# Kernel tuning notes

Hardware: AMD Instinct MI355X
Metric: run time of the kernel (lower is better)

The kernel has to match this reference:

```python
import jax, jax.numpy as jnp
import numpy as np

N = 50000; E = 800000; G = 256
FIN = 64; EIN = 16; HC = 128; H = 2; C = 64; EF = 64; NB = 2
EPS = 1e-5
SQRT_C = np.float32(np.sqrt(C))


def elu(x):
    return jax.nn.elu(x)


def seg_softmax(logits, seg, num):
    # numerically stable softmax over groups defined by seg
    m = jax.ops.segment_max(logits, seg, num_segments=num)
    e = jnp.exp(logits - m[seg])
    s = jax.ops.segment_sum(e, seg, num_segments=num)
    return e / s[seg]


def graph_ln(x, batch, gamma, beta):
    # PyG LayerNorm(mode='graph'): stats over all nodes AND channels of each graph
    cnt = jax.ops.segment_sum(jnp.ones((x.shape[0],), x.dtype), batch, num_segments=G) * x.shape[1]
    cnt = jnp.maximum(cnt, 1.0)
    s = jax.ops.segment_sum(x.sum(-1), batch, num_segments=G)
    ss = jax.ops.segment_sum((x * x).sum(-1), batch, num_segments=G)
    mean = s / cnt
    var = jnp.maximum(ss / cnt - mean * mean, 0.0)
    xn = (x - mean[batch][:, None]) * jax.lax.rsqrt(var + EPS)[batch][:, None]
    return xn * gamma + beta


def tconv(x, ea, src, dst, wq, bq, wk, bk, wv, bv, we, wsk, bsk):
    # PyG TransformerConv (concat=True, beta=False, root_weight=True, dropout=0)
    q = (x @ wq + bq).reshape(N, H, C)
    k = (x @ wk + bk).reshape(N, H, C)
    v = (x @ wv + bv).reshape(N, H, C)
    e = (ea @ we).reshape(E, H, C)
    kj = k[src] + e
    alpha = jnp.einsum('ehc,ehc->eh', q[dst], kj) / SQRT_C
    alpha = seg_softmax(alpha, dst, N)  # scatter-softmax over destination nodes
    out = jax.ops.segment_sum((v[src] + e) * alpha[:, :, None], dst, num_segments=N)
    return out.reshape(N, HC) + x @ wsk + bsk


def setup_inputs():
    key = jax.random.key(0)
    ks = jax.random.split(key, 16)
    rn = lambda k, shape, sc: jax.random.normal(k, shape, jnp.float32) * sc
    s64 = 1.0 / np.sqrt(64.0); s128 = 1.0 / np.sqrt(128.0); s16 = 1.0 / np.sqrt(16.0)
    return {
        'x': rn(ks[0], (N, FIN), 1.0),
        'edge_attr': rn(ks[1], (E, EIN), 1.0),
        'edge_index': jax.random.randint(ks[2], (2, E), 0, N, jnp.int32),
        'batch': jnp.sort(jax.random.randint(ks[3], (N,), 0, G, jnp.int32)),
        'w0': rn(ks[4], (FIN, HC), s64), 'b0': jnp.zeros((HC,), jnp.float32),
        'we0': rn(ks[5], (EIN, EF), s16), 'be0': jnp.zeros((EF,), jnp.float32),
        'ln0_g': jnp.ones((HC,), jnp.float32), 'ln0_b': jnp.zeros((HC,), jnp.float32),
        'qkv_w': rn(ks[6], (NB, 2, 3, HC, HC), s128), 'qkv_b': jnp.zeros((NB, 2, 3, HC), jnp.float32),
        'edge_w': rn(ks[7], (NB, 2, EF, HC), s64),
        'skip_w': rn(ks[8], (NB, 2, HC, HC), s128), 'skip_b': jnp.zeros((NB, 2, HC), jnp.float32),
        'up_w': rn(ks[9], (NB, 2, EF, EF), s64), 'up_b': jnp.zeros((NB, 2, EF), jnp.float32),
        'ng': jnp.ones((NB, 2, HC), jnp.float32), 'nb': jnp.zeros((NB, 2, HC), jnp.float32),
        'sag_wrel': rn(ks[10], (NB, HC), s128), 'sag_brel': jnp.zeros((NB,), jnp.float32),
        'sag_wroot': rn(ks[11], (NB, HC), s128),
        're_w': rn(ks[12], (NB, EF, HC), s64), 're_b': jnp.zeros((NB, HC), jnp.float32),
    }


def reference(x, edge_attr, edge_index, batch, w0, b0, we0, be0, ln0_g, ln0_b,
              qkv_w, qkv_b, edge_w, skip_w, skip_b, up_w, up_b, ng, nb,
              sag_wrel, sag_brel, sag_wroot, re_w, re_b):
    src, dst = edge_index[0], edge_index[1]
    h = elu(graph_ln(x @ w0 + b0, batch, ln0_g, ln0_b))
    ea = elu(edge_attr @ we0 + be0)
    embs = []
    for i in range(NB):
        # ne_update: conv1 + graph-LN + lin_up on edges
        h = tconv(h, ea, src, dst,
                  qkv_w[i, 0, 0], qkv_b[i, 0, 0], qkv_w[i, 0, 1], qkv_b[i, 0, 1],
                  qkv_w[i, 0, 2], qkv_b[i, 0, 2], edge_w[i, 0], skip_w[i, 0], skip_b[i, 0])
        h = elu(graph_ln(h, batch, ng[i, 0], nb[i, 0]))
        ea = elu(ea @ up_w[i, 0] + up_b[i, 0])
        # conv2 + lin_up2
        h = tconv(h, ea, src, dst,
                  qkv_w[i, 1, 0], qkv_b[i, 1, 0], qkv_w[i, 1, 1], qkv_b[i, 1, 1],
                  qkv_w[i, 1, 2], qkv_b[i, 1, 2], edge_w[i, 1], skip_w[i, 1], skip_b[i, 1])
        ea2 = ea @ up_w[i, 1] + up_b[i, 1]
        # SAGPooling(min_score=-1) keeps all nodes: score = per-graph softmax of GraphConv
        aggr = jax.ops.segment_sum(h[src], dst, num_segments=N)
        sc = aggr @ sag_wrel[i] + sag_brel[i] + h @ sag_wroot[i]  # [N]
        sc = seg_softmax(sc, batch, G)
        emb = jax.ops.segment_sum(h * sc[:, None], batch, num_segments=G)
        emb_e = elu(jax.ops.segment_sum(ea2, batch[src], num_segments=G) @ re_w[i] + re_b[i])
        emb = emb * emb_e
        emb = elu(emb / jnp.maximum(jnp.linalg.norm(emb, axis=1, keepdims=True), 1e-12))
        embs.append(emb)
        h = elu(graph_ln(h, batch, ng[i, 1], nb[i, 1]))
        ea = elu(ea2)
    return 0.6 * embs[0] + 0.4 * embs[-1]
```

## Files before the change

### kernel.cpp

```cpp
#include <hip/hip_runtime.h>
#include <math.h>

#define NN 50000
#define EE 800000
#define GG 256

typedef unsigned short u16;
typedef unsigned int u32;
typedef __attribute__((ext_vector_type(4))) float f32x4;
typedef __attribute__((ext_vector_type(8))) short bf16x8;

__device__ __forceinline__ float elu_f(float x) { return x > 0.f ? x : expm1f(x); }

__device__ __forceinline__ unsigned fenc(float f) {
  unsigned b = __float_as_uint(f);
  return (b & 0x80000000u) ? ~b : (b | 0x80000000u);
}
__device__ __forceinline__ float fdec(unsigned u) {
  return __uint_as_float((u & 0x80000000u) ? (u ^ 0x80000000u) : ~u);
}
__device__ __forceinline__ u16 f2b(float f) {
  u32 u = __float_as_uint(f);
  u32 r = (u + 0x7fffu + ((u >> 16) & 1u)) >> 16;
  return (u16)r;
// ... 90 lines not shown
  s[t] = v;
  __syncthreads();
  for (int off = 1; off < 256; off <<= 1) {
    int tmp = (t >= off) ? s[t - off] : 0;
    __syncthreads();
    s[t] += tmp;
    __syncthreads();
  }
  if (t < nb) bsum[t] = s[t] - v;
}

__global__ void scan3(const int* __restrict__ pre, const int* __restrict__ bsum,
                      const int* __restrict__ deg, int* __restrict__ row_start,
                      int* __restrict__ cursor, int n) {
  int i = blockIdx.x * 256 + threadIdx.x;
  if (i < n) {
    int v = pre[i] + bsum[blockIdx.x];
    row_start[i] = v;
    cursor[i] = v;
    if (i == n - 1) row_start[n] = v + deg[i];
  }
}

__global__ void gstart_build(const int* __restrict__ batch, int* __restrict__ gstart) {
  int n = blockIdx.x * blockDim.x + threadIdx.x;
  if (n > NN) return;
  int b = (n < NN) ? batch[n] : GG;
  int pb = (n == 0) ? -1 : batch[n - 1];
  for (int g = pb + 1; g <= b; ++g) gstart[g] = n;
}

__global__ void csr_pos(const int* __restrict__ src, const int* __restrict__ dst,
                        int* __restrict__ cursor, int* __restrict__ csr_src,
                        int* __restrict__ epos) {
  int e = blockIdx.x * blockDim.x + threadIdx.x;
  if (e >= EE) return;
  int pos = atomicAdd(&cursor[dst[e]], 1);
  csr_src[pos] = src[e];
  epos[e] = pos;
}

__global__ void out_hist(const int* __restrict__ csr_src, int* __restrict__ odeg) {
  int pos = blockIdx.x * blockDim.x + threadIdx.x;
  if (pos < EE) atomicAdd(&odeg[csr_src[pos]], 1);
}

__global__ void out_fill(const int* __restrict__ csr_src, int* __restrict__ ocursor,
                         int* __restrict__ operm) {
  int pos = blockIdx.x * blockDim.x + threadIdx.x;
  if (pos < EE) {
    int slot = atomicAdd(&ocursor[csr_src[pos]], 1);
    operm[slot] = pos;
  }
}

__global__ void sgstart_build(const int* __restrict__ out_start, const int* __restrict__ gstart,
                              int* __restrict__ sg_start) {
  int t = blockIdx.x * blockDim.x + threadIdx.x;
  if (t <= GG) sg_start[t] = out_start[gstart[t]];
}

__global__ void build_we0frag(const float* __restrict__ we0, u16* __restrict__ wf_hi,
                              u16* __restrict__ wf_lo) {
  int idx = blockIdx.x * 256 + threadIdx.x;
  if (idx >= 2048) return;
  int j = idx & 7, lane = (idx >> 3) & 63, t = idx >> 9;
  int k = (lane >> 4) * 8 + j;
  int c = t * 16 + (lane & 15);
  float w = (k < 16) ? we0[(size_t)k * 64 + c] : 0.f;
  u16 hi = f2b(w);
  wf_hi[idx] = hi;
  wf_lo[idx] = f2b(w - bf2f(hi));
}

__global__ __launch_bounds__(256) void ea_enc_mfma(const float* __restrict__ edge_attr,
                                                   const u16* __restrict__ wf_hi,
                                                   const u16* __restrict__ wf_lo,
                                                   const float* __restrict__ be0,
                                                   const int* __restrict__ epos,
                                                   u16* __restrict__ ea) {
  int lane = threadIdx.x & 63;
  int gwave = (blockIdx.x * 256 + threadIdx.x) >> 6;
  int nwaves = (gridDim.x * 256) >> 6;
  bf16x8 bh[4], bl[4];
#pragma unroll
  for (int t = 0; t < 4; ++t) {
    bh[t] = *reinterpret_cast<const bf16x8*>(wf_hi + ((size_t)(t * 64 + lane)) * 8);
    bl[t] = *reinterpret_cast<const bf16x8*>(wf_lo + ((size_t)(t * 64 + lane)) * 8);
  }
  float bias_c[4];
#pragma unroll
  for (int t = 0; t < 4; ++t) bias_c[t] = be0[t * 16 + (lane & 15)];
  const int rif = lane & 15;
  const int kg = lane >> 4;
  for (int mt = gwave; mt < EE / 16; mt += nwaves) {
    int base = mt * 16;
    bf16x8 ah = {}, al = {};
    if (kg < 2) {
      const float* ap = edge_attr + (size_t)(base + rif) * 16 + kg * 8;
      float4 f0 = *reinterpret_cast<const float4*>(ap);
      float4 f1 = *reinterpret_cast<const float4*>(ap + 4);
      float fv[8] = {f0.x, f0.y, f0.z, f0.w, f1.x, f1.y, f1.z, f1.w};
#pragma unroll
      for (int jj = 0; jj < 8; ++jj) {
        u16 hi = f2b(fv[jj]);
        ah[jj] = (short)hi;
        al[jj] = (short)f2b(fv[jj] - bf2f(hi));
      }
    }
    f32x4 acc[4] = {};
#pragma unroll
    for (int t = 0; t < 4; ++t) {
      acc[t] = __builtin_amdgcn_mfma_f32_16x16x32_bf16(ah, bh[t], acc[t], 0, 0, 0);
      acc[t] = __builtin_amdgcn_mfma_f32_16x16x32_bf16(ah, bl[t], acc[t], 0, 0, 0);
      acc[t] = __builtin_amdgcn_mfma_f32_16x16x32_bf16(al, bh[t], acc[t], 0, 0, 0);
    }
#pragma unroll
    for (int rg = 0; rg < 4; ++rg) {
      int pr = epos[base + kg * 4 + rg];
#pragma unroll
      for (int t = 0; t < 4; ++t)
        ea[(size_t)pr * 64 + t * 16 + rif] = f2b(elu_f(acc[t][rg] + bias_c[t]));
    }
  }
}

__global__ __launch_bounds__(256) void ln_stats_block(const float* __restrict__ h,
                                                      const int* __restrict__ gstart,
                                                      float* __restrict__ gmean,
                                                      float* __restrict__ grstd) {
  __shared__ float ls[4], lss[4];
  int g = blockIdx.x, t = threadIdx.x;
  int n0 = gstart[g], n1 = gstart[g + 1];
  int total4 = (n1 - n0) * 32;
  const float4* base = (const float4*)(h + (size_t)n0 * 128);
  float s = 0.f, ss = 0.f;
  for (int i = t; i < total4; i += 256) {
    float4 v = base[i];
    s += v.x + v.y + v.z + v.w;
    ss += v.x * v.x + v.y * v.y + v.z * v.z + v.w * v.w;
  }
  s = wred64(s);
  ss = wred64(ss);
  if ((t & 63) == 0) { ls[t >> 6] = s; lss[t >> 6] = ss; }
  __syncthreads();
  if (t == 0) {
    float S = ls[0] + ls[1] + ls[2] + ls[3];
    float SS = lss[0] + lss[1] + lss[2] + lss[3];
    float cnt = fmaxf((float)(n1 - n0) * 128.f, 1.0f);
    float mean = S / cnt;
    float var = fmaxf(SS / cnt - mean * mean, 0.f);
    gmean[g] = mean;
    grstd[g] = rsqrtf(var + 1e-5f);
  }
}

__global__ __launch_bounds__(256) void ln_apply(const float* __restrict__ in,
                                                u16* __restrict__ out_hi,
                                                u16* __restrict__ out_lo,
                                                const int* __restrict__ batch,
                                                const float* __restrict__ gmean,
                                                const float* __restrict__ grstd,
                                                const float* __restrict__ gamma,
                                                const float* __restrict__ beta) {
  int idx = blockIdx.x * blockDim.x + threadIdx.x;
  if (idx >= NN * 32) return;
  int n = idx >> 5, c4 = (idx & 31) * 4;
  int g = batch[n];
  float mean = gmean[g], rstd = grstd[g];
  float4 xv = *reinterpret_cast<const float4*>(in + (size_t)n * 128 + c4);
  float4 gv = *reinterpret_cast<const float4*>(gamma + c4);
  float4 bv = *reinterpret_cast<const float4*>(beta + c4);
  float v0 = elu_f((xv.x - mean) * rstd * gv.x + bv.x);
  float v1 = elu_f((xv.y - mean) * rstd * gv.y + bv.y);
  float v2 = elu_f((xv.z - mean) * rstd * gv.z + bv.z);
  float v3 = elu_f((xv.w - mean) * rstd * gv.w + bv.w);
  u16 h0 = f2b(v0), h1 = f2b(v1), h2 = f2b(v2), h3 = f2b(v3);
  uint2 hi = {(u32)h0 | ((u32)h1 << 16), (u32)h2 | ((u32)h3 << 16)};
  uint2 lo = {(u32)f2b(v0 - bf2f(h0)) | ((u32)f2b(v1 - bf2f(h1)) << 16),
              (u32)f2b(v2 - bf2f(h2)) | ((u32)f2b(v3 - bf2f(h3)) << 16)};
  *reinterpret_cast<uint2*>(out_hi + (size_t)n * 128 + c4) = hi;
  *reinterpret_cast<uint2*>(out_lo + (size_t)n * 128 + c4) = lo;
}

__global__ void build_wqe(const float* __restrict__ wq, const float* __restrict__ bq,
                          const float* __restrict__ we, float* __restrict__ WQE,
                          float* __restrict__ bqe) {
  int col = threadIdx.x;
  int row = blockIdx.x;
  int hh = col >> 6, j = col & 63;
  const float* wrow = (row < 128) ? (wq + (size_t)row * 128) : bq;
  float acc = 0.f;
  for (int c = 0; c < 64; ++c) acc += wrow[hh * 64 + c] * we[(size_t)j * 128 + hh * 64 + c];
  if (row < 128) WQE[(size_t)row * 128 + col] = acc;
  else bqe[col] = acc;
}

__global__ void build_wfrag2(const float* __restrict__ wq, const float* __restrict__ wk,
                             const float* __restrict__ wv, const float* __restrict__ WQE,
                             const float* __restrict__ wsk,
                             const float* __restrict__ bq, const float* __restrict__ bk,
                             const float* __restrict__ bv, const float* __restrict__ bqe,
                             const float* __restrict__ bsk,
                             u16* __restrict__ Wfrag_hi, u16* __restrict__ Wfrag_lo,
                             float* __restrict__ ball) {
  int idx = blockIdx.x * 256 + threadIdx.x;
  if (idx < 81920) {
    int j = idx & 7, lane = (idx >> 3) & 63, rest = idx >> 9;
    int tg = rest % 40, s = rest / 40;
    int k = s * 32 + (lane >> 4) * 8 + j;
    int col = tg * 16 + (lane & 15);
    int sel = col >> 7, c = col & 127;
    const float* src = sel == 0 ? wq : sel == 1 ? wk : sel == 2 ? wv : sel == 3 ? WQE : wsk;
    float w = src[(size_t)k * 128 + c];
    u16 hi = f2b(w);
    Wfrag_hi[idx] = hi;
    Wfrag_lo[idx] = f2b(w - bf2f(hi));
  }
  if (idx < 640) {
    int sel = idx >> 7, c = idx & 127;
    const float* s2 = sel == 0 ? bq : sel == 1 ? bk : sel == 2 ? bv : sel == 3 ? bqe : bsk;
    ball[idx] = s2[c];
  }
}

__global__ void build_wefrag(const float* __restrict__ we, u16* __restrict__ wef_hi,
                             u16* __restrict__ wef_lo) {
  int idx = blockIdx.x * 256 + threadIdx.x;
  if (idx >= 8192) return;
  int j = idx & 7, lane = (idx >> 3) & 63, rest = idx >> 9;
  int t = rest & 3, hh = (rest >> 2) & 1, s = rest >> 3;
  int k = s * 32 + (lane >> 4) * 8 + j;
  int col = hh * 64 + t * 16 + (lane & 15);
  float w = we[(size_t)k * 128 + col];
  u16 hi = f2b(w);
  wef_hi[idx] = hi;
  wef_lo[idx] = f2b(w - bf2f(hi));
}

__global__ void build_upfrag(const float* __restrict__ up, u16* __restrict__ upfrag) {
  int idx = blockIdx.x * 256 + threadIdx.x;
  if (idx >= 4096) return;
  int j = idx & 7, lane = (idx >> 3) & 63, st = idx >> 9;
  int s = st >> 2, t = st & 3;
  int k = s * 32 + (lane >> 4) * 8 + j;
  int c = t * 16 + (lane & 15);
  upfrag[idx] = f2b(up[k * 64 + c]);
}

__global__ void build_w2(const float* __restrict__ up, const float* __restrict__ ub,
                         const float* __restrict__ re_w, float* __restrict__ W2,
                         float* __restrict__ bvec) {
  int idx = blockIdx.x * 256 + threadIdx.x;
  if (idx < 64 * 128) {
    int k_ = idx >> 7, c = idx & 127;
    float a = 0.f;
    for (int j = 0; j < 64; ++j) a = fmaf(up[k_ * 64 + j], re_w[j * 128 + c], a);
    W2[idx] = a;
  } else if (idx < 64 * 128 + 128) {
    int c = idx - 64 * 128;
    float a = 0.f;
    for (int j = 0; j < 64; ++j) a = fmaf(ub[j], re_w[j * 128 + c], a);
    bvec[c] = a;
  }
}

__global__ __launch_bounds__(256) void node_gemm(const u16* __restrict__ h_hi,
                                                 const u16* __restrict__ h_lo,
                                                 const u16* __restrict__ Wfrag_hi,
                                                 const u16* __restrict__ Wfrag_lo,
                                                 const float* __restrict__ ball,
                                                 u16* __restrict__ nodebuf,
                                                 float* __restrict__ hn) {
  int tid = threadIdx.x;
  int lane = tid & 63;
  int wv = tid >> 6;
  int cb = blockIdx.x;
  int rbase = blockIdx.y * 64 + wv * 16;
  int rif = lane & 15, kg = lane >> 4;
  f32x4 acc[4] = {};
  int arow = rbase + rif;
  bool rowok = arow < NN;
  const u16* aph = h_hi + (size_t)arow * 128 + kg * 8;
  const u16* apl = h_lo + (size_t)arow * 128 + kg * 8;
#pragma unroll
  for (int s = 0; s < 4; ++s) {
    bf16x8 ah = {}, al = {};
    if (rowok) {
      ah = *reinterpret_cast<const bf16x8*>(aph + s * 32);
      al = *reinterpret_cast<const bf16x8*>(apl + s * 32);
    }
#pragma unroll
    for (int t = 0; t < 4; ++t) {
      size_t fo = ((size_t)((s * 40 + cb * 4 + t) * 64 + lane)) * 8;
      bf16x8 bh = *reinterpret_cast<const bf16x8*>(Wfrag_hi + fo);
      bf16x8 bl = *reinterpret_cast<const bf16x8*>(Wfrag_lo + fo);
      acc[t] = __builtin_amdgcn_mfma_f32_16x16x32_bf16(ah, bh, acc[t], 0, 0, 0);
      acc[t] = __builtin_amdgcn_mfma_f32_16x16x32_bf16(ah, bl, acc[t], 0, 0, 0);
      acc[t] = __builtin_amdgcn_mfma_f32_16x16x32_bf16(al, bh, acc[t], 0, 0, 0);
    }
  }
#pragma unroll
  for (int t = 0; t < 4; ++t) {
    int col = (cb * 4 + t) * 16 + rif;
    float bia = ball[col];
#pragma unroll
    for (int rg = 0; rg < 4; ++rg) {
      int row = rbase + kg * 4 + rg;
      if (row < NN) {
        float val = acc[t][rg] + bia;
        if (col < 512) {
          int idx;
          if (col < 128) idx = col;
          else if (col < 256) { int c1 = col - 128; idx = 256 + ((c1 >> 1) << 2) + (c1 & 1); }
          else if (col < 384) { int c2 = col - 256; idx = 256 + ((c2 >> 1) << 2) + 2 + (c2 & 1); }
          else idx = 128 + (col - 384);
          nodebuf[(size_t)row * 512 + idx] = f2b(val);
        } else {
          hn[(size_t)row * 128 + col - 512] = val;
        }
      }
    }
  }
}

__global__ __launch_bounds__(256) void edge_gemm(u16* __restrict__ ea,
                                                 const u16* __restrict__ upfrag,
                                                 const float* __restrict__ ub) {
  int lane = threadIdx.x & 63;
  int gwave = (blockIdx.x * 256 + threadIdx.x) >> 6;
  int nwaves = (gridDim.x * 256) >> 6;
  bf16x8 bfrag[2][4];
#pragma unroll
  for (int s = 0; s < 2; ++s)
#pragma unroll
    for (int t = 0; t < 4; ++t)
      bfrag[s][t] = *reinterpret_cast<const bf16x8*>(upfrag + ((size_t)((s * 4 + t) * 64 + lane)) * 8);
  float bias_c[4];
#pragma unroll
  for (int t = 0; t < 4; ++t) bias_c[t] = ub[t * 16 + (lane & 15)];
  const int rif = lane & 15;
  const int kg = lane >> 4;
  for (int mt = gwave; mt < EE / 16; mt += nwaves) {
    size_t rowbase = (size_t)mt * 16;
    const u16* arow = ea + (rowbase + rif) * 64;
    bf16x8 a0 = *reinterpret_cast<const bf16x8*>(arow + kg * 8);
    bf16x8 a1 = *reinterpret_cast<const bf16x8*>(arow + 32 + kg * 8);
    f32x4 acc[4] = {};
#pragma unroll
    for (int t = 0; t < 4; ++t) {
      acc[t] = __builtin_amdgcn_mfma_f32_16x16x32_bf16(a0, bfrag[0][t], acc[t], 0, 0, 0);
      acc[t] = __builtin_amdgcn_mfma_f32_16x16x32_bf16(a1, bfrag[1][t], acc[t], 0, 0, 0);
    }
#pragma unroll
    for (int t = 0; t < 4; ++t)
#pragma unroll
      for (int rg = 0; rg < 4; ++rg) {
        float val = acc[t][rg] + bias_c[t];
        ea[(rowbase + kg * 4 + rg) * 64 + t * 16 + rif] = f2b(elu_f(val));
      }
  }
}

__global__ __launch_bounds__(256) void bd_gemm(const u16* __restrict__ r_hi,
                                               const u16* __restrict__ r_lo,
                                               const u16* __restrict__ wef_hi,
                                               const u16* __restrict__ wef_lo,
                                               float* __restrict__ hn) {
  int tid = threadIdx.x;
  int lane = tid & 63;
  int w = blockIdx.x * 4 + (tid >> 6);
  if (w >= NN / 16) return;
  int rif = lane & 15, kg = lane >> 4;
  size_t rowbase = (size_t)w * 16;
  const u16* ahb = r_hi + (rowbase + rif) * 128;
  const u16* alb = r_lo + (rowbase + rif) * 128;
  f32x4 acc[2][4] = {};
#pragma unroll
  for (int hh = 0; hh < 2; ++hh)
#pragma unroll
    for (int s = 0; s < 2; ++s) {
      int ko = hh * 64 + s * 32 + kg * 8;
      bf16x8 ah = *reinterpret_cast<const bf16x8*>(ahb + ko);
      bf16x8 al = *reinterpret_cast<const bf16x8*>(alb + ko);
#pragma unroll
      for (int t = 0; t < 4; ++t) {
        size_t fo = ((size_t)((((s * 2 + hh) * 4 + t)) * 64 + lane)) * 8;
        bf16x8 bh = *reinterpret_cast<const bf16x8*>(wef_hi + fo);
        bf16x8 bl = *reinterpret_cast<const bf16x8*>(wef_lo + fo);
        acc[hh][t] = __builtin_amdgcn_mfma_f32_16x16x32_bf16(ah, bh, acc[hh][t], 0, 0, 0);
        acc[hh][t] = __builtin_amdgcn_mfma_f32_16x16x32_bf16(ah, bl, acc[hh][t], 0, 0, 0);
        acc[hh][t] = __builtin_amdgcn_mfma_f32_16x16x32_bf16(al, bh, acc[hh][t], 0, 0, 0);
      }
    }
#pragma unroll
  for (int hh = 0; hh < 2; ++hh)
#pragma unroll
    for (int t = 0; t < 4; ++t)
#pragma unroll
      for (int rg = 0; rg < 4; ++rg) {
        size_t row = rowbase + kg * 4 + rg;
        int col = hh * 64 + t * 16 + rif;
        hn[row * 128 + col] += acc[hh][t][rg];
      }
}

__global__ __launch_bounds__(256) void gsum_pre(const u16* __restrict__ ea,
                                                const int* __restrict__ sg_start,
                                                const int* __restrict__ sg_perm,
                                                float* __restrict__ gsum_in) {
  __shared__ float red[8][64];
  int g = blockIdx.x, t = threadIdx.x;
  int c2 = t & 31;
  int rgrp = t >> 5;
  int gr = blockIdx.y * 8 + rgrp;
  int p0 = sg_start[g], p1 = sg_start[g + 1];
  float slo = 0.f, shi = 0.f;
  for (int i = p0 + gr; i < p1; i += 128) {
    int pos = sg_perm[i];
    u32 w = ((const u32*)ea)[(size_t)pos * 32 + c2];
    slo += lo2f(w);
    shi += hi2f(w);
  }
  red[rgrp][c2 * 2] = slo;
  red[rgrp][c2 * 2 + 1] = shi;
  __syncthreads();
  if (t < 64) {
    float a = 0.f;
#pragma unroll
    for (int rr = 0; rr < 8; ++rr) a += red[rr][t];
    atomicAdd(&gsum_in[(size_t)g * 64 + t], a);
  }
}

__global__ void emb_e_kernel(const float* __restrict__ gsum_in, const int* __restrict__ sg_start,
                             const float* __restrict__ W2, const float* __restrict__ bvec,
                             const float* __restrict__ re_b, float* __restrict__ embE) {
  int g = blockIdx.x, c = threadIdx.x;
  float cnt = (float)(sg_start[g + 1] - sg_start[g]);
  float a = re_b[c] + cnt * bvec[c];
  for (int k_ = 0; k_ < 64; ++k_) a = fmaf(gsum_in[(size_t)g * 64 + k_], W2[k_ * 128 + c], a);
  embE[(size_t)g * 128 + c] = elu_f(a);
}

__global__ __launch_bounds__(256) void attn_node(const u32* __restrict__ nodebuf,
                                                 const u16* __restrict__ ea,
                                                 const int* __restrict__ row_start,
                                                 const int* __restrict__ csr_src,
                                                 float* __restrict__ hn,
                                                 u32* __restrict__ r_hi,
                                                 u32* __restrict__ r_lo) {
  int d = (blockIdx.x * blockDim.x + threadIdx.x) >> 6;
  if (d >= NN) return;
  int lane = threadIdx.x & 63;
  int p0 = row_start[d], p1 = row_start[d + 1];
  if (p0 == p1) {
    r_hi[(size_t)d * 64 + lane] = 0u;
    r_lo[(size_t)d * 64 + lane] = 0u;
    return;
  }
  int cnt = p1 - p0;
  size_t dbase = (size_t)d * 256;
  u32 qv = nodebuf[dbase + lane];
  u32 qev = nodebuf[dbase + 64 + lane];
  const int lea = lane & 31;
  float mA = -3.4e38f, sA = 0.f, a0A = 0.f, a1A = 0.f, r0A = 0.f, r1A = 0.f;
  float mB = -3.4e38f, sB = 0.f, a0B = 0.f, a1B = 0.f, r0B = 0.f, r1B = 0.f;
  int sa = csr_src[p0];
  uint2 kvA = *((const uint2*)(nodebuf + (size_t)sa * 256 + 128) + lane);
  u32 eaA = ((const u32*)ea)[(size_t)p0 * 32 + lea];
  int pB0 = (cnt > 1) ? p0 + 1 : p0;
  int sb = csr_src[pB0];
  uint2 kvB = *((const uint2*)(nodebuf + (size_t)sb * 256 + 128) + lane);
  u32 eaB = ((const u32*)ea)[(size_t)pB0 * 32 + lea];
  for (int i = 0; i < cnt; i += 2) {
    int ni = i + 2;
    int nA = (ni < cnt) ? p0 + ni : p0;
    int nB = (ni + 1 < cnt) ? p0 + ni + 1 : p0;
    int sa2 = csr_src[nA];
    uint2 kvA2 = *((const uint2*)(nodebuf + (size_t)sa2 * 256 + 128) + lane);
    u32 eaA2 = ((const u32*)ea)[(size_t)nA * 32 + lea];
    int sb2 = csr_src[nB];
    uint2 kvB2 = *((const uint2*)(nodebuf + (size_t)sb2 * 256 + 128) + lane);
    u32 eaB2 = ((const u32*)ea)[(size_t)nB * 32 + lea];
    float pA = lo2f(qv) * lo2f(kvA.x) + hi2f(qv) * hi2f(kvA.x) +
               lo2f(qev) * lo2f(eaA) + hi2f(qev) * hi2f(eaA);
    float pB = lo2f(qv) * lo2f(kvB.x) + hi2f(qv) * hi2f(kvB.x) +
               lo2f(qev) * lo2f(eaB) + hi2f(qev) * hi2f(eaB);
#pragma unroll
    for (int mm = 16; mm; mm >>= 1) {
      pA += __shfl_xor(pA, mm, 64);
      pB += __shfl_xor(pB, mm, 64);
    }
    {
      float l = pA * 0.125f;
      float mn = fmaxf(mA, l);
      float f = __expf(mA - mn), w = __expf(l - mn);
      sA = sA * f + w;
      a0A = a0A * f + w * lo2f(kvA.y); a1A = a1A * f + w * hi2f(kvA.y);
      r0A = r0A * f + w * lo2f(eaA);   r1A = r1A * f + w * hi2f(eaA);
      mA = mn;
    }
    if (i + 1 < cnt) {
      float l = pB * 0.125f;
      float mn = fmaxf(mB, l);
      float f = __expf(mB - mn), w = __expf(l - mn);
      sB = sB * f + w;
      a0B = a0B * f + w * lo2f(kvB.y); a1B = a1B * f + w * hi2f(kvB.y);
      r0B = r0B * f + w * lo2f(eaB);   r1B = r1B * f + w * hi2f(eaB);
      mB = mn;
    }
    kvA = kvA2; eaA = eaA2; kvB = kvB2; eaB = eaB2;
  }
  float mn = fmaxf(mA, mB);
  float fA = __expf(mA - mn);
  float fB = (cnt > 1) ? __expf(mB - mn) : 0.f;
  float ssum = sA * fA + sB * fB;
  float a0 = a0A * fA + a0B * fB, a1 = a1A * fA + a1B * fB;
  float r0 = r0A * fA + r0B * fB, r1 = r1A * fA + r1B * fB;
  float inv = 1.f / ssum;
  size_t ob = (size_t)d * 128 + lane * 2;
  hn[ob] += a0 * inv;
  hn[ob + 1] += a1 * inv;
  float rv0 = r0 * inv, rv1 = r1 * inv;
  u16 h0 = f2b(rv0), h1 = f2b(rv1);
  r_hi[(size_t)d * 64 + lane] = (u32)h0 | ((u32)h1 << 16);
  r_lo[(size_t)d * 64 + lane] = (u32)f2b(rv0 - bf2f(h0)) | ((u32)f2b(rv1 - bf2f(h1)) << 16);
}

__global__ __launch_bounds__(256) void node_dots(const float* __restrict__ hn,
                                                 const float* __restrict__ wrel,
                                                 const float* __restrict__ wroot,
                                                 float* __restrict__ hrel,
                                                 float* __restrict__ troot) {
  int n = (blockIdx.x * blockDim.x + threadIdx.x) >> 6;
  if (n >= NN) return;
  int lane = threadIdx.x & 63;
  float x0 = hn[(size_t)n * 128 + lane], x1 = hn[(size_t)n * 128 + 64 + lane];
  float tr = wred64(x0 * wrel[lane] + x1 * wrel[64 + lane]);
  float tt = wred64(x0 * wroot[lane] + x1 * wroot[64 + lane]);
  if (lane == 0) { hrel[n] = tr; troot[n] = tt; }
}

__global__ __launch_bounds__(256) void sag_gather(const float* __restrict__ hrel,
                                                  const float* __restrict__ troot,
                                                  const float* __restrict__ brel,
                                                  const int* __restrict__ row_start,
                                                  const int* __restrict__ csr_src,
                                                  const int* __restrict__ batch,
                                                  float* __restrict__ sc, unsigned* __restrict__ gm) {
  int n = blockIdx.x * blockDim.x + threadIdx.x;
  if (n >= NN) return;
  float s = 0.f;
  int p1 = row_start[n + 1];
  for (int pos = row_start[n]; pos < p1; ++pos) s += hrel[csr_src[pos]];
  float v = s + troot[n] + brel[0];
  sc[n] = v;
  atomicMax(&gm[batch[n]], fenc(v));
}

__global__ __launch_bounds__(256) void sag_exp(const float* __restrict__ sc,
                                               const int* __restrict__ batch,
                                               const unsigned* __restrict__ gm,
                                               float* __restrict__ gs, float* __restrict__ scp) {
  int n = blockIdx.x * blockDim.x + threadIdx.x;
  if (n >= NN) return;
  int g = batch[n];
  float p = __expf(sc[n] - fdec(gm[g]));
  scp[n] = p;
  atomicAdd(&gs[g], p);
}

__global__ void emb_block(const float* __restrict__ hn, const float* __restrict__ scp,
                          const float* __restrict__ gs, const int* __restrict__ gstart,
                          const float* __restrict__ embE, float* __restrict__ dstv) {
  __shared__ float part[2];
  int g = blockIdx.x, c = threadIdx.x;
  int n0 = gstart[g], n1 = gstart[g + 1];
  float invg = 1.f / gs[g];
  float acc = 0.f;
  for (int n = n0; n < n1; ++n) acc = fmaf(hn[(size_t)n * 128 + c], scp[n] * invg, acc);
  float val = acc * embE[(size_t)g * 128 + c];
  float sq = val * val;
#pragma unroll
  for (int mm = 32; mm; mm >>= 1) sq += __shfl_xor(sq, mm, 64);
  if ((c & 63) == 0) part[c >> 6] = sq;
  __syncthreads();
  float nrm = sqrtf(part[0] + part[1]);
  dstv[(size_t)g * 128 + c] = elu_f(val / fmaxf(nrm, 1e-12f));
}

__global__ void final_combine(const float* __restrict__ e0, const float* __restrict__ e1,
                              float* __restrict__ out) {
  int idx = blockIdx.x * blockDim.x + threadIdx.x;
  if (idx >= GG * 128) return;
  out[idx] = 0.6f * e0[idx] + 0.4f * e1[idx];
}

extern "C" void kernel_launch(void* const* d_in, const int* in_sizes, int n_in,
                              void* d_out, int out_size, void* d_ws, size_t ws_size,
                              hipStream_t stream) {
  const float* x = (const float*)d_in[0];
  const float* edge_attr = (const float*)d_in[1];
  const int* edge_index = (const int*)d_in[2];
  const int* batch = (const int*)d_in[3];
  const float* w0 = (const float*)d_in[4];
  const float* b0 = (const float*)d_in[5];
  const float* we0 = (const float*)d_in[6];
  const float* be0 = (const float*)d_in[7];
  const float* ln0_g = (const float*)d_in[8];
  const float* ln0_b = (const float*)d_in[9];
  const float* qkv_w = (const float*)d_in[10];
  const float* qkv_b = (const float*)d_in[11];
  const float* edge_w = (const float*)d_in[12];
  const float* skip_w = (const float*)d_in[13];
  const float* skip_b = (const float*)d_in[14];
  const float* up_w = (const float*)d_in[15];
  const float* up_b = (const float*)d_in[16];
  const float* ng = (const float*)d_in[17];
  const float* nbeta = (const float*)d_in[18];
  const float* sag_wrel = (const float*)d_in[19];
  const float* sag_brel = (const float*)d_in[20];
  const float* sag_wroot = (const float*)d_in[21];
  const float* re_w = (const float*)d_in[22];
  const float* re_b = (const float*)d_in[23];
  const int* srcp = edge_index;
  const int* dstp = edge_index + EE;
  float* out = (float*)d_out;
  (void)in_sizes; (void)n_in;

  float* ws = (float*)d_ws;
  size_t o = 0;
  auto alloc = [&](size_t n) { n = (n + 3) & ~(size_t)3; float* p = ws + o; o += n; return p; };
  u16* h_hi = (u16*)alloc((size_t)NN * 64);
  u16* h_lo = (u16*)alloc((size_t)NN * 64);
  float* hn = alloc((size_t)NN * 128);
  u32* r_hi = (u32*)alloc((size_t)NN * 64);
  u32* r_lo = (u32*)alloc((size_t)NN * 64);
  u16* nodebuf = (u16*)alloc((size_t)NN * 256);
  u16* ea = (u16*)alloc((size_t)EE * 32);
  int* csr_src = (int*)alloc(EE);
  int* epos = (int*)alloc(EE);
  int* deg = (int*)alloc(NN);
  int* pre = (int*)alloc(NN);
  int* bsum = (int*)alloc(256);
  int* row_start = (int*)alloc(NN + 1);
  int* cursor = (int*)alloc(NN);
  int* out_start = (int*)alloc(NN + 1);
  int* gstart = (int*)alloc(GG + 1);
  int* sg_perm = (int*)alloc(EE);
  int* sg_start = (int*)alloc(GG + 1);
  float* gsum_in = alloc(GG * 64);
  float* W2 = alloc(64 * 128);
  float* bvec = alloc(128);
  u16* upfrag = (u16*)alloc(2048);
  u16* Wfrag_hi = (u16*)alloc(40960);
  u16* Wfrag_lo = (u16*)alloc(40960);
  u16* wef_hi = (u16*)alloc(4096);
  u16* wef_lo = (u16*)alloc(4096);
  u16* wef0_hi = (u16*)alloc(1024);
  u16* wef0_lo = (u16*)alloc(1024);
  unsigned* gm = (unsigned*)alloc(GG);
  float* gs = alloc(GG);
  float* gmean = alloc(GG);
  float* grstd = alloc(GG);
  float* WQE = alloc(128 * 128);
  float* bqe = alloc(128);
  float* ball = alloc(640);
  float* hrel = alloc(NN);
  float* troot = alloc(NN);
  float* sc = alloc(NN);
  float* scp = alloc(NN);
  float* embE = alloc(GG * 128);
  float* embs0 = alloc(GG * 128);
  float* embs1 = alloc(GG * 128);

  const size_t need = o * sizeof(float);
  if (ws_size < need) {
    hipMemsetAsync(d_out, 0, (size_t)out_size * sizeof(float), stream);
    return;
  }
  const int NSCAN = (NN + 255) / 256;

  auto gemm = [&](const float* A, const float* B, const float* bias, float* C,
                  int M, int Nn, int K, int act, int accum) {
    dim3 g((Nn + 63) / 64, (M + 63) / 64);
    gemm_kernel<<<g, 256, 0, stream>>>(A, B, bias, C, M, Nn, K, act, accum);
  };
  auto ex_scan = [&](const int* degp, int* startp, int* curp) {
    scan1<<<NSCAN, 256, 0, stream>>>(degp, pre, bsum, NN);
    scan2<<<1, 256, 0, stream>>>(bsum, NSCAN);
    scan3<<<NSCAN, 256, 0, stream>>>(pre, bsum, degp, startp, curp, NN);
  };
  auto graph_ln = [&](const float* in, const float* gamma, const float* beta) {
    ln_stats_block<<<GG, 256, 0, stream>>>(in, gstart, gmean, grstd);
    ln_apply<<<NN * 32 / 256, 256, 0, stream>>>(in, h_hi, h_lo, batch, gmean, grstd, gamma, beta);
  };
  auto tconv = [&](int il) {
    const float* wq = qkv_w + (size_t)(il * 3 + 0) * 128 * 128;
    const float* wk = qkv_w + (size_t)(il * 3 + 1) * 128 * 128;
    const float* wv = qkv_w + (size_t)(il * 3 + 2) * 128 * 128;
    const float* bq = qkv_b + (il * 3 + 0) * 128;
    const float* bk = qkv_b + (il * 3 + 1) * 128;
    const float* bv = qkv_b + (il * 3 + 2) * 128;
    const float* we = edge_w + (size_t)il * 64 * 128;
    const float* wsk = skip_w + (size_t)il * 128 * 128;
    const float* bsk = skip_b + il * 128;
    build_wqe<<<129, 128, 0, stream>>>(wq, bq, we, WQE, bqe);
    build_wfrag2<<<320, 256, 0, stream>>>(wq, wk, wv, WQE, wsk, bq, bk, bv, bqe, bsk,
                                          Wfrag_hi, Wfrag_lo, ball);
    build_wefrag<<<32, 256, 0, stream>>>(we, wef_hi, wef_lo);
    dim3 ng2(10, (NN + 63) / 64);
    node_gemm<<<ng2, 256, 0, stream>>>(h_hi, h_lo, Wfrag_hi, Wfrag_lo, ball, nodebuf, hn);
    attn_node<<<NN / 4, 256, 0, stream>>>((const u32*)nodebuf, ea, row_start, csr_src, hn,
                                          r_hi, r_lo);
    bd_gemm<<<(NN / 16 + 3) / 4, 256, 0, stream>>>((const u16*)r_hi, (const u16*)r_lo,
                                                   wef_hi, wef_lo, hn);
  };
  auto ea_mlp = [&](int il) {
    build_upfrag<<<16, 256, 0, stream>>>(up_w + (size_t)il * 4096, upfrag);
    edge_gemm<<<2048, 256, 0, stream>>>(ea, upfrag, up_b + il * 64);
  };

  hipMemsetAsync(deg, 0, NN * sizeof(int), stream);
  csr_hist<<<(EE + 255) / 256, 256, 0, stream>>>(dstp, deg);
  ex_scan(deg, row_start, cursor);
  gstart_build<<<(NN + 256) / 256, 256, 0, stream>>>(batch, gstart);
  csr_pos<<<(EE + 255) / 256, 256, 0, stream>>>(srcp, dstp, cursor, csr_src, epos);
  build_we0frag<<<8, 256, 0, stream>>>(we0, wef0_hi, wef0_lo);
  ea_enc_mfma<<<2048, 256, 0, stream>>>(edge_attr, wef0_hi, wef0_lo, be0, epos, ea);
  hipMemsetAsync(deg, 0, NN * sizeof(int), stream);
  out_hist<<<(EE + 255) / 256, 256, 0, stream>>>(csr_src, deg);
  ex_scan(deg, out_start, cursor);
  out_fill<<<(EE + 255) / 256, 256, 0, stream>>>(csr_src, cursor, sg_perm);
  sgstart_build<<<2, 256, 0, stream>>>(out_start, gstart, sg_start);
  gemm(x, w0, b0, hn, NN, 128, 64, 0, 0);
  graph_ln(hn, ln0_g, ln0_b);

  for (int i = 0; i < 2; ++i) {
    tconv(i * 2 + 0);
    graph_ln(hn, ng + (i * 2) * 128, nbeta + (i * 2) * 128);
    ea_mlp(i * 2);
    tconv(i * 2 + 1);
    hipMemsetAsync(gm, 0, 2 * GG * sizeof(float), stream);
    hipMemsetAsync(gsum_in, 0, GG * 64 * sizeof(float), stream);
    dim3 gsg(GG, 16);
    gsum_pre<<<gsg, 256, 0, stream>>>(ea, sg_start, sg_perm, gsum_in);
    build_w2<<<33, 256, 0, stream>>>(up_w + (size_t)(i * 2 + 1) * 4096,
                                     up_b + (i * 2 + 1) * 64,
                                     re_w + (size_t)i * 64 * 128, W2, bvec);
    if (i == 0) ea_mlp(i * 2 + 1);
    node_dots<<<NN / 4, 256, 0, stream>>>(hn, sag_wrel + i * 128, sag_wroot + i * 128, hrel, troot);
    sag_gather<<<(NN + 255) / 256, 256, 0, stream>>>(hrel, troot, sag_brel + i, row_start,
                                                     csr_src, batch, sc, gm);
    sag_exp<<<(NN + 255) / 256, 256, 0, stream>>>(sc, batch, gm, gs, scp);
    emb_e_kernel<<<GG, 128, 0, stream>>>(gsum_in, sg_start, W2, bvec, re_b + i * 128, embE);
    emb_block<<<GG, 128, 0, stream>>>(hn, scp, gs, gstart, embE, i == 0 ? embs0 : embs1);
    if (i == 0) graph_ln(hn, ng + (i * 2 + 1) * 128, nbeta + (i * 2 + 1) * 128);
  }
  final_combine<<<GG * 128 / 256, 256, 0, stream>>>(embs0, embs1, out);
}
```

Measured before the change: 1.764 ms.

## Fuse graph-norm stats into bd_gemm epilogue and merge setup kernels

```diff
diff --git a/kernel.cpp b/kernel.cpp
--- a/kernel.cpp
+++ b/kernel.cpp
@@ -266,6 +266,18 @@
     float var = fmaxf(SS / cnt - mean * mean, 0.f);
     gmean[g] = mean;
     grstd[g] = rsqrtf(var + 1e-5f);
+  }
+}
+
+__global__ void ln_final2(const float* __restrict__ gstat, const int* __restrict__ gstart,
+                          float* __restrict__ gmean, float* __restrict__ grstd) {
+  int t = threadIdx.x;
+  if (t < GG) {
+    float cnt = fmaxf((float)(gstart[t + 1] - gstart[t]) * 128.f, 1.0f);
+    float mean = gstat[t] / cnt;
+    float var = fmaxf(gstat[GG + t] / cnt - mean * mean, 0.f);
+    gmean[t] = mean;
+    grstd[t] = rsqrtf(var + 1e-5f);
   }
 }
 
@@ -312,12 +324,13 @@
 
 __global__ void build_wfrag2(const float* __restrict__ wq, const float* __restrict__ wk,
                              const float* __restrict__ wv, const float* __restrict__ WQE,
-                             const float* __restrict__ wsk,
+                             const float* __restrict__ wsk, const float* __restrict__ we,
                              const float* __restrict__ bq, const float* __restrict__ bk,
                              const float* __restrict__ bv, const float* __restrict__ bqe,
                              const float* __restrict__ bsk,
                              u16* __restrict__ Wfrag_hi, u16* __restrict__ Wfrag_lo,
-                             float* __restrict__ ball) {
+                             u16* __restrict__ wef_hi, u16* __restrict__ wef_lo,
+                             float* __restrict__ ball, float* __restrict__ gstat) {
   int idx = blockIdx.x * 256 + threadIdx.x;
   if (idx < 81920) {
     int j = idx & 7, lane = (idx >> 3) & 63, rest = idx >> 9;
@@ -330,26 +343,24 @@
     u16 hi = f2b(w);
     Wfrag_hi[idx] = hi;
     Wfrag_lo[idx] = f2b(w - bf2f(hi));
+  } else if (idx < 90112) {
+    int i2 = idx - 81920;
+    int j = i2 & 7, lane = (i2 >> 3) & 63, rest = i2 >> 9;
+    int t = rest & 3, hh = (rest >> 2) & 1, s = rest >> 3;
+    int k = s * 32 + (lane >> 4) * 8 + j;
+    int col = hh * 64 + t * 16 + (lane & 15);
+    float w = we[(size_t)k * 128 + col];
+    u16 hi = f2b(w);
+    wef_hi[i2] = hi;
+    wef_lo[i2] = f2b(w - bf2f(hi));
+  } else if (idx < 90112 + 2 * GG) {
+    gstat[idx - 90112] = 0.f;
   }
   if (idx < 640) {
     int sel = idx >> 7, c = idx & 127;
     const float* s2 = sel == 0 ? bq : sel == 1 ? bk : sel == 2 ? bv : sel == 3 ? bqe : bsk;
     ball[idx] = s2[c];
   }
-}
-
-__global__ void build_wefrag(const float* __restrict__ we, u16* __restrict__ wef_hi,
-                             u16* __restrict__ wef_lo) {
-  int idx = blockIdx.x * 256 + threadIdx.x;
-  if (idx >= 8192) return;
-  int j = idx & 7, lane = (idx >> 3) & 63, rest = idx >> 9;
-  int t = rest & 3, hh = (rest >> 2) & 1, s = rest >> 3;
-  int k = s * 32 + (lane >> 4) * 8 + j;
-  int col = hh * 64 + t * 16 + (lane & 15);
-  float w = we[(size_t)k * 128 + col];
-  u16 hi = f2b(w);
-  wef_hi[idx] = hi;
-  wef_lo[idx] = f2b(w - bf2f(hi));
 }
 
 __global__ void build_upfrag(const float* __restrict__ up, u16* __restrict__ upfrag) {
@@ -364,7 +375,7 @@
 
 __global__ void build_w2(const float* __restrict__ up, const float* __restrict__ ub,
                          const float* __restrict__ re_w, float* __restrict__ W2,
-                         float* __restrict__ bvec) {
+                         float* __restrict__ bvec, float* __restrict__ gsum_in) {
   int idx = blockIdx.x * 256 + threadIdx.x;
   if (idx < 64 * 128) {
     int k_ = idx >> 7, c = idx & 127;
@@ -377,6 +388,7 @@
     for (int j = 0; j < 64; ++j) a = fmaf(ub[j], re_w[j * 128 + c], a);
     bvec[c] = a;
   }
+  if (idx < GG * 64) gsum_in[idx] = 0.f;
 }
 
 __global__ __launch_bounds__(256) void node_gemm(const u16* __restrict__ h_hi,
@@ -480,7 +492,9 @@
                                                const u16* __restrict__ r_lo,
                                                const u16* __restrict__ wef_hi,
                                                const u16* __restrict__ wef_lo,
-                                               float* __restrict__ hn) {
+                                               float* __restrict__ hn,
+                                               const int* __restrict__ batch,
+                                               float* __restrict__ gstat) {
   int tid = threadIdx.x;
   int lane = tid & 63;
   int w = blockIdx.x * 4 + (tid >> 6);
@@ -508,15 +522,30 @@
       }
     }
 #pragma unroll
-  for (int hh = 0; hh < 2; ++hh)
-#pragma unroll
-    for (int t = 0; t < 4; ++t)
-#pragma unroll
-      for (int rg = 0; rg < 4; ++rg) {
-        size_t row = rowbase + kg * 4 + rg;
-        int col = hh * 64 + t * 16 + rif;
-        hn[row * 128 + col] += acc[hh][t][rg];
+  for (int rg = 0; rg < 4; ++rg) {
+    size_t row = rowbase + kg * 4 + rg;
+    float s = 0.f, sq = 0.f;
+#pragma unroll
+    for (int hh = 0; hh < 2; ++hh)
+#pragma unroll
+      for (int t = 0; t < 4; ++t) {
+        size_t off = row * 128 + hh * 64 + t * 16 + rif;
+        float val = hn[off] + acc[hh][t][rg];
+        hn[off] = val;
+        s += val;
+        sq += val * val;
       }
+#pragma unroll
+    for (int mm = 1; mm <= 8; mm <<= 1) {
+      s += __shfl_xor(s, mm, 64);
+      sq += __shfl_xor(sq, mm, 64);
+    }
+    if (rif == 0) {
+      int g = batch[row];
+      atomicAdd(&gstat[g], s);
+      atomicAdd(&gstat[GG + g], sq);
+    }
+  }
 }
 
 __global__ __launch_bounds__(256) void gsum_pre(const u16* __restrict__ ea,
@@ -557,8 +586,8 @@
   embE[(size_t)g * 128 + c] = elu_f(a);
 }
 
-__global__ __launch_bounds__(256) void attn_node(const u32* __restrict__ nodebuf,
-                                                 const u16* __restrict__ ea,
+__global__ __launch_bounds__(256) void attn_node(const u32* __restrict__ nb32,
+                                                 const u32* __restrict__ ea32,
                                                  const int* __restrict__ row_start,
                                                  const int* __restrict__ csr_src,
                                                  float* __restrict__ hn,
@@ -567,87 +596,99 @@
   int d = (blockIdx.x * blockDim.x + threadIdx.x) >> 6;
   if (d >= NN) return;
   int lane = threadIdx.x & 63;
+  int half = lane >> 5;
+  int l = lane & 31;
+  int li = l & 15;
+  int qi = (l >> 4) * 32 + li * 2;
   int p0 = row_start[d], p1 = row_start[d + 1];
   if (p0 == p1) {
-    r_hi[(size_t)d * 64 + lane] = 0u;
-    r_lo[(size_t)d * 64 + lane] = 0u;
+    if (!half) {
+      uint2 z = {0u, 0u};
+      *reinterpret_cast<uint2*>(r_hi + (size_t)d * 64 + qi) = z;
+      *reinterpret_cast<uint2*>(r_lo + (size_t)d * 64 + qi) = z;
+    }
     return;
   }
+  size_t dbase = (size_t)d * 256;
+  uint2 qp = *reinterpret_cast<const uint2*>(nb32 + dbase + qi);
+  uint2 qep = *reinterpret_cast<const uint2*>(nb32 + dbase + 64 + qi);
+  float q0 = lo2f(qp.x), q1 = hi2f(qp.x), q2 = lo2f(qp.y), q3 = hi2f(qp.y);
+  float g0 = lo2f(qep.x), g1 = hi2f(qep.x), g2 = lo2f(qep.y), g3 = hi2f(qep.y);
   int cnt = p1 - p0;
-  size_t dbase = (size_t)d * 256;
-  u32 qv = nodebuf[dbase + lane];
-  u32 qev = nodebuf[dbase + 64 + lane];
-  const int lea = lane & 31;
-  float mA = -3.4e38f, sA = 0.f, a0A = 0.f, a1A = 0.f, r0A = 0.f, r1A = 0.f;
-  float mB = -3.4e38f, sB = 0.f, a0B = 0.f, a1B = 0.f, r0B = 0.f, r1B = 0.f;
-  int sa = csr_src[p0];
-  uint2 kvA = *((const uint2*)(nodebuf + (size_t)sa * 256 + 128) + lane);
-  u32 eaA = ((const u32*)ea)[(size_t)p0 * 32 + lea];
-  int pB0 = (cnt > 1) ? p0 + 1 : p0;
-  int sb = csr_src[pB0];
-  uint2 kvB = *((const uint2*)(nodebuf + (size_t)sb * 256 + 128) + lane);
-  u32 eaB = ((const u32*)ea)[(size_t)pB0 * 32 + lea];
-  for (int i = 0; i < cnt; i += 2) {
-    int ni = i + 2;
-    int nA = (ni < cnt) ? p0 + ni : p0;
-    int nB = (ni + 1 < cnt) ? p0 + ni + 1 : p0;
-    int sa2 = csr_src[nA];
-    uint2 kvA2 = *((const uint2*)(nodebuf + (size_t)sa2 * 256 + 128) + lane);
-    u32 eaA2 = ((const u32*)ea)[(size_t)nA * 32 + lea];
-    int sb2 = csr_src[nB];
-    uint2 kvB2 = *((const uint2*)(nodebuf + (size_t)sb2 * 256 + 128) + lane);
-    u32 eaB2 = ((const u32*)ea)[(size_t)nB * 32 + lea];
-    float pA = lo2f(qv) * lo2f(kvA.x) + hi2f(qv) * hi2f(kvA.x) +
-               lo2f(qev) * lo2f(eaA) + hi2f(qev) * hi2f(eaA);
-    float pB = lo2f(qv) * lo2f(kvB.x) + hi2f(qv) * hi2f(kvB.x) +
-               lo2f(qev) * lo2f(eaB) + hi2f(qev) * hi2f(eaB);
-#pragma unroll
-    for (int mm = 16; mm; mm >>= 1) {
-      pA += __shfl_xor(pA, mm, 64);
-      pB += __shfl_xor(pB, mm, 64);
-    }
-    {
-      float l = pA * 0.125f;
-      float mn = fmaxf(mA, l);
-      float f = __expf(mA - mn), w = __expf(l - mn);
-      sA = sA * f + w;
-      a0A = a0A * f + w * lo2f(kvA.y); a1A = a1A * f + w * hi2f(kvA.y);
-      r0A = r0A * f + w * lo2f(eaA);   r1A = r1A * f + w * hi2f(eaA);
-      mA = mn;
-    }
-    if (i + 1 < cnt) {
-      float l = pB * 0.125f;
-      float mn = fmaxf(mB, l);
-      float f = __expf(mB - mn), w = __expf(l - mn);
-      sB = sB * f + w;
-      a0B = a0B * f + w * lo2f(kvB.y); a1B = a1B * f + w * hi2f(kvB.y);
-      r0B = r0B * f + w * lo2f(eaB);   r1B = r1B * f + w * hi2f(eaB);
-      mB = mn;
-    }
-    kvA = kvA2; eaA = eaA2; kvB = kvB2; eaB = eaB2;
-  }
-  float mn = fmaxf(mA, mB);
-  float fA = __expf(mA - mn);
-  float fB = (cnt > 1) ? __expf(mB - mn) : 0.f;
-  float ssum = sA * fA + sB * fB;
-  float a0 = a0A * fA + a0B * fB, a1 = a1A * fA + a1B * fB;
-  float r0 = r0A * fA + r0B * fB, r1 = r1A * fA + r1B * fB;
-  float inv = 1.f / ssum;
-  size_t ob = (size_t)d * 128 + lane * 2;
-  hn[ob] += a0 * inv;
-  hn[ob + 1] += a1 * inv;
-  float rv0 = r0 * inv, rv1 = r1 * inv;
-  u16 h0 = f2b(rv0), h1 = f2b(rv1);
-  r_hi[(size_t)d * 64 + lane] = (u32)h0 | ((u32)h1 << 16);
-  r_lo[(size_t)d * 64 + lane] = (u32)f2b(rv0 - bf2f(h0)) | ((u32)f2b(rv1 - bf2f(h1)) << 16);
+  int nIter = (cnt + 1) >> 1;
+  float m = -3.4e38f, ss = 0.f;
+  float a0 = 0.f, a1 = 0.f, a2 = 0.f, a3 = 0.f;
+  float r0 = 0.f, r1 = 0.f, r2 = 0.f, r3 = 0.f;
+  int i = half;
+  bool vld = i < cnt;
+  int pc = vld ? p0 + i : p0;
+  int sc = csr_src[pc];
+  uint4 kv = *reinterpret_cast<const uint4*>(nb32 + (size_t)sc * 256 + 128 + qi * 2);
+  uint2 ev = *reinterpret_cast<const uint2*>(ea32 + (size_t)pc * 32 + li * 2);
+  for (int j = 0; j < nIter; ++j) {
+    int i2 = i + 2;
+    bool nvld = i2 < cnt;
+    int pn = nvld ? p0 + i2 : p0;
+    int sn = csr_src[pn];
+    uint4 kvn = *reinterpret_cast<const uint4*>(nb32 + (size_t)sn * 256 + 128 + qi * 2);
+    uint2 evn = *reinterpret_cast<const uint2*>(ea32 + (size_t)pn * 32 + li * 2);
+    float x0 = lo2f(ev.x), x1 = hi2f(ev.x), x2 = lo2f(ev.y), x3 = hi2f(ev.y);
+    float p = q0 * lo2f(kv.x) + q1 * hi2f(kv.x) + q2 * lo2f(kv.z) + q3 * hi2f(kv.z) +
+              g0 * x0 + g1 * x1 + g2 * x2 + g3 * x3;
+#pragma unroll
+    for (int mm = 1; mm <= 8; mm <<= 1) p += __shfl_xor(p, mm, 64);
+    float lg = vld ? p * 0.125f : -3.4e38f;
+    float mn = fmaxf(m, lg);
+    float f = __expf(m - mn), w = __expf(lg - mn);
+    ss = ss * f + w;
+    a0 = a0 * f + w * lo2f(kv.y); a1 = a1 * f + w * hi2f(kv.y);
+    a2 = a2 * f + w * lo2f(kv.w); a3 = a3 * f + w * hi2f(kv.w);
+    r0 = r0 * f + w * x0; r1 = r1 * f + w * x1;
+    r2 = r2 * f + w * x2; r3 = r3 * f + w * x3;
+    m = mn;
+    i = i2; vld = nvld; kv = kvn; ev = evn;
+  }
+  float mo = __shfl_xor(m, 32, 64);
+  float so = __shfl_xor(ss, 32, 64);
+  float b0 = __shfl_xor(a0, 32, 64), b1 = __shfl_xor(a1, 32, 64);
+  float b2 = __shfl_xor(a2, 32, 64), b3 = __shfl_xor(a3, 32, 64);
+  float t0 = __shfl_xor(r0, 32, 64), t1 = __shfl_xor(r1, 32, 64);
+  float t2 = __shfl_xor(r2, 32, 64), t3 = __shfl_xor(r3, 32, 64);
+  float mn = fmaxf(m, mo);
+  float fs = __expf(m - mn), fo = __expf(mo - mn);
+  ss = ss * fs + so * fo;
+  a0 = a0 * fs + b0 * fo; a1 = a1 * fs + b1 * fo;
+  a2 = a2 * fs + b2 * fo; a3 = a3 * fs + b3 * fo;
+  r0 = r0 * fs + t0 * fo; r1 = r1 * fs + t1 * fo;
+  r2 = r2 * fs + t2 * fo; r3 = r3 * fs + t3 * fo;
+  if (!half) {
+    float inv = 1.f / ss;
+    int ch0 = (l >> 4) * 64 + li * 4;
+    float* hp = hn + (size_t)d * 128 + ch0;
+    float4 hv = *reinterpret_cast<float4*>(hp);
+    hv.x += a0 * inv; hv.y += a1 * inv; hv.z += a2 * inv; hv.w += a3 * inv;
+    *reinterpret_cast<float4*>(hp) = hv;
+    float rv0 = r0 * inv, rv1 = r1 * inv, rv2 = r2 * inv, rv3 = r3 * inv;
+    u16 h0 = f2b(rv0), h1 = f2b(rv1), h2 = f2b(rv2), h3 = f2b(rv3);
+    uint2 rh = {(u32)h0 | ((u32)h1 << 16), (u32)h2 | ((u32)h3 << 16)};
+    uint2 rl = {(u32)f2b(rv0 - bf2f(h0)) | ((u32)f2b(rv1 - bf2f(h1)) << 16),
+                (u32)f2b(rv2 - bf2f(h2)) | ((u32)f2b(rv3 - bf2f(h3)) << 16)};
+    *reinterpret_cast<uint2*>(r_hi + (size_t)d * 64 + qi) = rh;
+    *reinterpret_cast<uint2*>(r_lo + (size_t)d * 64 + qi) = rl;
+  }
 }
 
 __global__ __launch_bounds__(256) void node_dots(const float* __restrict__ hn,
                                                  const float* __restrict__ wrel,
                                                  const float* __restrict__ wroot,
                                                  float* __restrict__ hrel,
-                                                 float* __restrict__ troot) {
-  int n = (blockIdx.x * blockDim.x + threadIdx.x) >> 6;
+                                                 float* __restrict__ troot,
+                                                 unsigned* __restrict__ gm,
+                                                 float* __restrict__ gs) {
+  int tid0 = blockIdx.x * blockDim.x + threadIdx.x;
+  if (tid0 < GG) gm[tid0] = 0u;
+  else if (tid0 < 2 * GG) gs[tid0 - GG] = 0.f;
+  int n = tid0 >> 6;
   if (n >= NN) return;
   int lane = threadIdx.x & 63;
   float x0 = hn[(size_t)n * 128 + lane], x1 = hn[(size_t)n * 128 + 64 + lane];
@@ -776,6 +817,7 @@
   u16* wef0_lo = (u16*)alloc(1024);
   unsigned* gm = (unsigned*)alloc(GG);
   float* gs = alloc(GG);
+  float* gstat = alloc(2 * GG);
   float* gmean = alloc(GG);
   float* grstd = alloc(GG);
   float* WQE = alloc(128 * 128);
@@ -806,10 +848,6 @@
     scan2<<<1, 256, 0, stream>>>(bsum, NSCAN);
     scan3<<<NSCAN, 256, 0, stream>>>(pre, bsum, degp, startp, curp, NN);
   };
-  auto graph_ln = [&](const float* in, const float* gamma, const float* beta) {
-    ln_stats_block<<<GG, 256, 0, stream>>>(in, gstart, gmean, grstd);
-    ln_apply<<<NN * 32 / 256, 256, 0, stream>>>(in, h_hi, h_lo, batch, gmean, grstd, gamma, beta);
-  };
   auto tconv = [&](int il) {
     const float* wq = qkv_w + (size_t)(il * 3 + 0) * 128 * 128;
     const float* wk = qkv_w + (size_t)(il * 3 + 1) * 128 * 128;
@@ -821,15 +859,18 @@
     const float* wsk = skip_w + (size_t)il * 128 * 128;
     const float* bsk = skip_b + il * 128;
     build_wqe<<<129, 128, 0, stream>>>(wq, bq, we, WQE, bqe);
-    build_wfrag2<<<320, 256, 0, stream>>>(wq, wk, wv, WQE, wsk, bq, bk, bv, bqe, bsk,
-                                          Wfrag_hi, Wfrag_lo, ball);
-    build_wefrag<<<32, 256, 0, stream>>>(we, wef_hi, wef_lo);
+    build_wfrag2<<<354, 256, 0, stream>>>(wq, wk, wv, WQE, wsk, we, bq, bk, bv, bqe, bsk,
+                                          Wfrag_hi, Wfrag_lo, wef_hi, wef_lo, ball, gstat);
     dim3 ng2(10, (NN + 63) / 64);
     node_gemm<<<ng2, 256, 0, stream>>>(h_hi, h_lo, Wfrag_hi, Wfrag_lo, ball, nodebuf, hn);
-    attn_node<<<NN / 4, 256, 0, stream>>>((const u32*)nodebuf, ea, row_start, csr_src, hn,
-                                          r_hi, r_lo);
+    attn_node<<<NN / 4, 256, 0, stream>>>((const u32*)nodebuf, (const u32*)ea, row_start,
+                                          csr_src, hn, r_hi, r_lo);
     bd_gemm<<<(NN / 16 + 3) / 4, 256, 0, stream>>>((const u16*)r_hi, (const u16*)r_lo,
-                                                   wef_hi, wef_lo, hn);
+                                                   wef_hi, wef_lo, hn, batch, gstat);
+  };
+  auto graph_ln_fast = [&](const float* gamma, const float* beta) {
+    ln_final2<<<1, 256, 0, stream>>>(gstat, gstart, gmean, grstd);
+    ln_apply<<<NN * 32 / 256, 256, 0, stream>>>(hn, h_hi, h_lo, batch, gmean, grstd, gamma, beta);
   };
   auto ea_mlp = [&](int il) {
     build_upfrag<<<16, 256, 0, stream>>>(up_w + (size_t)il * 4096, upfrag);
@@ -849,28 +890,28 @@
   out_fill<<<(EE + 255) / 256, 256, 0, stream>>>(csr_src, cursor, sg_perm);
   sgstart_build<<<2, 256, 0, stream>>>(out_start, gstart, sg_start);
   gemm(x, w0, b0, hn, NN, 128, 64, 0, 0);
-  graph_ln(hn, ln0_g, ln0_b);
+  ln_stats_block<<<GG, 256, 0, stream>>>(hn, gstart, gmean, grstd);
+  ln_apply<<<NN * 32 / 256, 256, 0, stream>>>(hn, h_hi, h_lo, batch, gmean, grstd, ln0_g, ln0_b);
 
   for (int i = 0; i < 2; ++i) {
     tconv(i * 2 + 0);
-    graph_ln(hn, ng + (i * 2) * 128, nbeta + (i * 2) * 128);
+    graph_ln_fast(ng + (i * 2) * 128, nbeta + (i * 2) * 128);
     ea_mlp(i * 2);
     tconv(i * 2 + 1);
-    hipMemsetAsync(gm, 0, 2 * GG * sizeof(float), stream);
-    hipMemsetAsync(gsum_in, 0, GG * 64 * sizeof(float), stream);
+    build_w2<<<64, 256, 0, stream>>>(up_w + (size_t)(i * 2 + 1) * 4096,
+                                     up_b + (i * 2 + 1) * 64,
+                                     re_w + (size_t)i * 64 * 128, W2, bvec, gsum_in);
     dim3 gsg(GG, 16);
     gsum_pre<<<gsg, 256, 0, stream>>>(ea, sg_start, sg_perm, gsum_in);
-    build_w2<<<33, 256, 0, stream>>>(up_w + (size_t)(i * 2 + 1) * 4096,
-                                     up_b + (i * 2 + 1) * 64,
-                                     re_w + (size_t)i * 64 * 128, W2, bvec);
     if (i == 0) ea_mlp(i * 2 + 1);
-    node_dots<<<NN / 4, 256, 0, stream>>>(hn, sag_wrel + i * 128, sag_wroot + i * 128, hrel, troot);
+    node_dots<<<NN / 4, 256, 0, stream>>>(hn, sag_wrel + i * 128, sag_wroot + i * 128,
+                                          hrel, troot, gm, gs);
     sag_gather<<<(NN + 255) / 256, 256, 0, stream>>>(hrel, troot, sag_brel + i, row_start,
                                                      csr_src, batch, sc, gm);
     sag_exp<<<(NN + 255) / 256, 256, 0, stream>>>(sc, batch, gm, gs, scp);
     emb_e_kernel<<<GG, 128, 0, stream>>>(gsum_in, sg_start, W2, bvec, re_b + i * 128, embE);
     emb_block<<<GG, 128, 0, stream>>>(hn, scp, gs, gstart, embE, i == 0 ? embs0 : embs1);
-    if (i == 0) graph_ln(hn, ng + (i * 2 + 1) * 128, nbeta + (i * 2 + 1) * 128);
+    if (i == 0) graph_ln_fast(ng + (i * 2 + 1) * 128, nbeta + (i * 2 + 1) * 128);
   }
   final_combine<<<GG * 128 / 256, 256, 0, stream>>>(embs0, embs1, out);
 }
```

New measurement: 2.088 ms. 18.4% more time.
